# Kernel tuning notes

Measured on AMD Instinct MI355X. Metric: run time of the kernel, lower is better.

Reference implementation:

```python
import jax, jax.numpy as jnp
import numpy as np

N = 20000          # num proposals (nodes)
E = 320000         # num edges
IN = 4096          # roi feature dim
EMB = 200          # glove embed dim
HID = 512          # hidden dim
NH = 8             # heads (conv1)
HC = HID // NH     # 64 per-head channels
NCLS = 151         # VG object classes
NEG_SLOPE = 0.2    # PyG GATConv leaky_relu slope


def setup_inputs() -> dict:
    key = jax.random.key(0)
    ks = jax.random.split(key, 18)
    d_in1 = IN + EMB + 128  # 4424, conv1 input dim
    inp = {
        "roi_features": jax.random.normal(ks[0], (N, IN), jnp.float32),
        "box_info": jax.random.uniform(ks[1], (N, 9), jnp.float32),
        # embedding tables
        "emb1": jax.random.normal(ks[2], (NCLS, EMB), jnp.float32) * 0.02,
        "emb2": jax.random.normal(ks[3], (NCLS, EMB), jnp.float32) * 0.02,
        # bbox MLP 9 -> 32 -> 128
        "bw1": jax.random.normal(ks[4], (9, 32), jnp.float32) / np.sqrt(9),
        "bb1": jnp.zeros((32,), jnp.float32),
        "bw2": jax.random.normal(ks[5], (32, 128), jnp.float32) / np.sqrt(32),
        "bb2": jnp.zeros((128,), jnp.float32),
        # GATConv1: d_in1 -> 8 heads x 64, concat
        "W1": jax.random.normal(ks[6], (d_in1, NH * HC), jnp.float32) / np.sqrt(d_in1),
        "a_src1": jax.random.normal(ks[7], (NH, HC), jnp.float32) * 0.1,
        "a_dst1": jax.random.normal(ks[8], (NH, HC), jnp.float32) * 0.1,
        "bias1": jnp.zeros((NH * HC,), jnp.float32),
        # GATConv2: 512 -> 512, 1 head, concat=False
        "W2": jax.random.normal(ks[9], (HID, HID), jnp.float32) / np.sqrt(HID),
        "a_src2": jax.random.normal(ks[10], (1, HID), jnp.float32) * 0.1,
        "a_dst2": jax.random.normal(ks[11], (1, HID), jnp.float32) * 0.1,
        "bias2": jnp.zeros((HID,), jnp.float32),
        # int inputs
        "obj_labels": jax.random.randint(ks[12], (N,), 0, NCLS, jnp.int32),
        "edge_index": jax.random.randint(ks[13], (2, E), 0, N, jnp.int32),
    }
    return inp


def _segment_softmax(logits, seg, n):
    # logits: [E, H]; softmax over edges sharing the same destination seg id
    m = jax.ops.segment_max(logits, seg, num_segments=n)
    e = jnp.exp(logits - m[seg])
    s = jax.ops.segment_sum(e, seg, num_segments=n)
    return e / (s[seg] + 1e-16)


def _gat_conv(x, src, dst, W, a_src, a_dst, bias, concat):
    # PyG GATConv (self-loops already included in src/dst); dropout off (eval)
    n = x.shape[0]
    H, C = a_src.shape
    h = (x @ W).reshape(n, H, C)                      # [N, H, C]
    al_s = jnp.einsum('nhc,hc->nh', h, a_src)         # [N, H]
    al_d = jnp.einsum('nhc,hc->nh', h, a_dst)
    logits = jax.nn.leaky_relu(al_s[src] + al_d[dst], NEG_SLOPE)  # [E, H]
    alpha = _segment_softmax(logits, dst, n)          # [E, H]
    out = jax.ops.segment_sum(alpha[:, :, None] * h[src], dst, num_segments=n)
    out = out.reshape(n, H * C) if concat else out.mean(axis=1)
    return out + bias


def reference(roi_features, box_info, emb1, emb2, bw1, bb1, bw2, bb2,
              W1, a_src1, a_dst1, bias1, W2, a_src2, a_dst2, bias2,
              obj_labels, edge_index):
    n = roi_features.shape[0]
    # predcls mode: GT labels -> embedding lookup
    obj_embed = emb1[obj_labels]                              # [N, 200]
    pos = jax.nn.relu(box_info @ bw1 + bb1)
    pos = jax.nn.relu(pos @ bw2 + bb2)                        # [N, 128]
    x = jnp.concatenate([roi_features, obj_embed, pos], -1)  # [N, 4424]

    # add self-loops (PyG GATConv default)
    ar = jnp.arange(n, dtype=edge_index.dtype)
    src = jnp.concatenate([edge_index[0], ar])
    dst = jnp.concatenate([edge_index[1], ar])

    edge_f1 = jax.nn.elu(_gat_conv(x, src, dst, W1, a_src1, a_dst1, bias1, True))
    obj_feats = _gat_conv(edge_f1, src, dst, W2, a_src2, a_dst2, bias2, False)

    obj_dists = jax.nn.one_hot(obj_labels, NCLS, dtype=jnp.float32)
    edge_pre_rep = jnp.concatenate([roi_features, obj_feats, emb2[obj_labels]], -1)
    return obj_dists, obj_labels, edge_pre_rep
```

## Files before the change

kernel.cpp:

```cpp
#include <hip/hip_runtime.h>
#include <hip/hip_bf16.h>

#define NNODES 20000
#define NEDGES 320000
#define ETOT   (NEDGES + NNODES)
#define KPADX  4224
#define SK     4
#define KC     (KPADX / SK)
#define MPAD   20096
#define NCLS   151
#define EPRW   4808
#define OUT_LAB_OFF  3020000L
#define OUT_EPR_OFF  3040000L
#define NSLOPE 0.2f

typedef __attribute__((ext_vector_type(8))) short bf16x8;
typedef __attribute__((ext_vector_type(4))) float f32x4;
typedef __attribute__((ext_vector_type(4))) short s16x4;

__device__ __forceinline__ short f2bf(float v) {
  union { __hip_bfloat16 b; short s; } u;
  u.b = __float2bfloat16(v);
  return u.s;
}

__device__ __forceinline__ float bf2f(short s) {
  union { float f; unsigned u; } x;
  x.u = ((unsigned)(unsigned short)s) << 16;
  return x.f;
}

__device__ __forceinline__ void gld16(const short* g, short* l) {
  __builtin_amdgcn_global_load_lds(
      (const __attribute__((address_space(1))) unsigned int*)g,
      (__attribute__((address_space(3))) unsigned int*)l, 16, 0, 0);
}

#define QB0  5000
#define QB0b (QB0 + 10000)
#define QB1  (QB0b + 5000)
#define QB2  (QB1 + 1584)
#define QB3  (QB2 + 2112)
#define QB4  (QB3 + 256)
#define QB5  (QB4 + 1329)
#define QB6  (QB5 + 151)

__global__ __launch_bounds__(256) void mega_prep_kernel(
    const float* __restrict__ roi, const float* __restrict__ box,
    const float* __restrict__ emb1, const float* __restrict__ emb2,
    const float* __restrict__ bw1, const float* __restrict__ bb1,
    const float* __restrict__ bw2, const float* __restrict__ bb2,
    const float* __restrict__ W1, const float* __restrict__ W2,
    const int* __restrict__ labels, const int* __restrict__ ei,
    short* __restrict__ x, short* __restrict__ w1t, short* __restrict__ w2t,
    short* __restrict__ ef1, int* __restrict__ deg,
    float* __restrict__ als2, float* __restrict__ ald2,
    float* __restrict__ E1, float* __restrict__ dout) {
  const int b = blockIdx.x;
  const int tid = threadIdx.x;

  __shared__ float hids[4][32];
  __shared__ float tile[32][33];

  if (b < QB0) {
    const int c0 = b * 2048 + tid;
    f32x4 v0[8], v1[8];
#pragma unroll
    for (int k = 0; k < 8; ++k) {
      const int c = c0 + k * 256;
      const float* src = &roi[((long)(c >> 9) << 12) + (c & 511) * 8];
      v0[k] = *(const f32x4*)src;
      v1[k] = *(const f32x4*)(src + 4);
    }
#pragma unroll
    for (int k = 0; k < 8; ++k) {
      const int c = c0 + k * 256;
      bf16x8 bb;
      bb[0] = f2bf(v0[k].x); bb[1] = f2bf(v0[k].y);
      bb[2] = f2bf(v0[k].z); bb[3] = f2bf(v0[k].w);
      bb[4] = f2bf(v1[k].x); bb[5] = f2bf(v1[k].y);
      bb[6] = f2bf(v1[k].z); bb[7] = f2bf(v1[k].w);
      __builtin_nontemporal_store(bb,
          (bf16x8*)&x[(long)(c >> 9) * KPADX + (c & 511) * 8]);
    }
  } else if (b < QB0b) {
    const int t = b - QB0;
    const int c0 = t * 2048 + tid;
    f32x4 v[8];
#pragma unroll
    for (int k = 0; k < 8; ++k) {
      const int c = c0 + k * 256;
      v[k] = *(const f32x4*)&roi[((long)(c >> 10) << 12) + (c & 1023) * 4];
    }
#pragma unroll
    for (int k = 0; k < 8; ++k) {
      const int c = c0 + k * 256;
      __builtin_nontemporal_store(v[k],
          (f32x4*)&dout[OUT_EPR_OFF + (long)(c >> 10) * EPRW + (c & 1023) * 4]);
    }
  } else if (b < QB1) {
    const int w = tid >> 6;
    const int lane = tid & 63;
    const int nd = (b - QB0b) * 4 + w;
    if (lane < 32) {
      float a = bb1[lane];
#pragma unroll
      for (int i = 0; i < 9; ++i) a += box[nd * 9 + i] * bw1[i * 32 + lane];
      hids[w][lane] = a > 0.f ? a : 0.f;
    }
    __syncthreads();
    const long xrow = (long)nd * KPADX;
#pragma unroll
    for (int jj = 0; jj < 2; ++jj) {
      const int j = lane + jj * 64;
      float a = bb2[j];
#pragma unroll
      for (int i = 0; i < 32; ++i) a += hids[w][i] * bw2[i * 128 + j];
      a = a > 0.f ? a : 0.f;
      x[xrow + 4096 + j] = f2bf(a);
    }
    const int lab = labels[nd];
    float* epr = dout + OUT_EPR_OFF + (long)nd * EPRW;
    if (lane < 50) {
      const f32x4 e2 = *(const f32x4*)&emb2[lab * 200 + lane * 4];
      __builtin_nontemporal_store(e2, (f32x4*)&epr[4608 + lane * 4]);
    }
    for (int j = lane; j < NCLS; j += 64)
      dout[(long)nd * NCLS + j] = (j == lab) ? 1.f : 0.f;
    if (lane == 0) dout[OUT_LAB_OFF + nd] = (float)lab;
  } else if (b < QB2) {
    const int t = (b - QB1) * 256 + tid;
    if (t < 96 * KPADX) x[(long)NNODES * KPADX + t] = 0;
    if (t < 96 * 512)   ef1[(long)NNODES * 512 + t] = 0;
    if (t < MPAD)       { als2[t] = 0.f; ald2[t] = 0.f; }
  } else if (b < QB3) {
    const int t = b - QB2;
    const int n0 = (t % 16) * 32;
    const int k0 = (t / 16) * 32;
    const int tx = tid & 31, ty = tid >> 5;
#pragma unroll
    for (int i = ty; i < 32; i += 8) {
      const int kp = k0 + i;
      const int src = kp < 4096 ? kp : kp + 200;
      tile[i][tx] = W1[(long)src * 512 + (n0 + tx)];
    }
    __syncthreads();
#pragma unroll
    for (int i = ty; i < 32; i += 8)
      w1t[(long)(n0 + i) * KPADX + (k0 + tx)] = f2bf(tile[tx][i]);
  } else if (b < QB4) {
    const int t = b - QB3;
    const int n0 = (t % 16) * 32;
    const int k0 = (t / 16) * 32;
    const int tx = tid & 31, ty = tid >> 5;
#pragma unroll
    for (int i = ty; i < 32; i += 8)
      tile[i][tx] = W2[(long)(k0 + i) * 512 + (n0 + tx)];
    __syncthreads();
#pragma unroll
    for (int i = ty; i < 32; i += 8)
      w2t[(long)(n0 + i) * 512 + (k0 + tx)] = f2bf(tile[tx][i]);
  } else if (b < QB5) {
    const int e = (b - QB4) * 256 + tid;
    if (e < ETOT) {
      const int d = (e < NEDGES) ? ei[NEDGES + e] : (e - NEDGES);
      atomicAdd(&deg[d], 1);
    }
  } else {
    const int c = b - QB5;
#pragma unroll
    for (int jj = 0; jj < 2; ++jj) {
      const int j = tid + jj * 256;
      float a = 0.f;
      for (int k = 0; k < 200; ++k)
        a += emb1[c * 200 + k] * W1[(long)(4096 + k) * 512 + j];
      E1[c * 512 + j] = a;
    }
  }
}

__global__ __launch_bounds__(256) void scan_kernel(const int* __restrict__ deg,
                                                   int* __restrict__ off,
                                                   int* __restrict__ cur) {
  __shared__ int part[256];
  const int tid = threadIdx.x;
  const int chunk = (NNODES + 255) / 256;
  int start = tid * chunk;
  int end = start + chunk; if (end > NNODES) end = NNODES;
  int s = 0;
  for (int i = start; i < end; ++i) s += deg[i];
  part[tid] = s;
  __syncthreads();
  for (int d = 1; d < 256; d <<= 1) {
    const int v = (tid >= d) ? part[tid - d] : 0;
    __syncthreads();
    part[tid] += v;
    __syncthreads();
  }
  int base = part[tid] - s;
  for (int i = start; i < end; ++i) { off[i] = base; cur[i] = base; base += deg[i]; }
}

__global__ void csr_fill_kernel(const int* __restrict__ ei, int* __restrict__ cur,
                                int* __restrict__ csrs) {
  const int e = blockIdx.x * 256 + threadIdx.x;
  if (e >= ETOT) return;
  const int s = (e < NEDGES) ? ei[e] : (e - NEDGES);
  const int d = (e < NEDGES) ? ei[NEDGES + e] : (e - NEDGES);
  unsigned slot = (unsigned)atomicAdd(&cur[d], 1);
  if (slot >= ETOT) slot = 0;
  csrs[slot] = s;
}

__global__ __launch_bounds__(256) void gemm_split(const short* __restrict__ A,
                                                  const short* __restrict__ BT,
                                                  short* __restrict__ hp) {
  __shared__ short As[2][4096];
  __shared__ short Bs[2][4096];
  const int tid = threadIdx.x;
  const int lane = tid & 63;
  const int w = tid >> 6;
  const int wr = w >> 1, wc = w & 1;
  const int wid = (blockIdx.x & 7) * 314 + ((int)blockIdx.x >> 3);
  const long bm = (long)(wid >> 4) * 128;
  const int  sk = (wid >> 2) & 3;
  const long bn = (long)(wid & 3) * 128;

  f32x4 acc[4][4] = {};

  const short* gA0 = A + (bm + w * 32 + (lane >> 2)) * (long)KPADX + sk * KC + (lane & 3) * 8;
  const short* gA1 = gA0 + 16L * KPADX;
  const short* gB0 = BT + (bn + w * 32 + (lane >> 2)) * (long)KPADX + sk * KC + (lane & 3) * 8;
  const short* gB1 = gB0 + 16L * KPADX;

  const int lofs = w * 1024;
  const int ar = (wr * 64 + (lane & 15)) * 32 + (lane >> 4) * 8;
  const int br = (wc * 64 + (lane & 15)) * 32 + (lane >> 4) * 8;

  gld16(gA0, &As[0][lofs]); gld16(gA1, &As[0][lofs + 512]);
  gld16(gB0, &Bs[0][lofs]); gld16(gB1, &Bs[0][lofs + 512]);
  gA0 += 32; gA1 += 32; gB0 += 32; gB1 += 32;

  const int NT = KC / 32;
  int cur = 0;
  for (int t = 0; t < NT; ++t) {
    if (t + 1 < NT) {
      gld16(gA0, &As[cur ^ 1][lofs]); gld16(gA1, &As[cur ^ 1][lofs + 512]);
      gld16(gB0, &Bs[cur ^ 1][lofs]); gld16(gB1, &Bs[cur ^ 1][lofs + 512]);
      gA0 += 32; gA1 += 32; gB0 += 32; gB1 += 32;
      asm volatile("s_waitcnt vmcnt(4)" ::: "memory");
    } else {
      asm volatile("s_waitcnt vmcnt(0)" ::: "memory");
    }
    __builtin_amdgcn_s_barrier();
    bf16x8 a[4], b[4];
#pragma unroll
    for (int mi = 0; mi < 4; ++mi) a[mi] = *(const bf16x8*)&As[cur][ar + mi * 512];
#pragma unroll
    for (int ni = 0; ni < 4; ++ni) b[ni] = *(const bf16x8*)&Bs[cur][br + ni * 512];
#pragma unroll
    for (int mi = 0; mi < 4; ++mi)
#pragma unroll
      for (int ni = 0; ni < 4; ++ni)
        acc[mi][ni] = __builtin_amdgcn_mfma_f32_16x16x32_bf16(a[mi], b[ni], acc[mi][ni], 0, 0, 0);
    __builtin_amdgcn_s_barrier();
    cur ^= 1;
  }

  short* Cp = hp + (long)sk * MPAD * 512;
#pragma unroll
  for (int mi = 0; mi < 4; ++mi) {
#pragma unroll
    for (int ni = 0; ni < 4; ++ni) {
      const long row0 = bm + wr * 64 + mi * 16 + (lane >> 4) * 4;
      const long col  = bn + wc * 64 + ni * 16 + (lane & 15);
#pragma unroll
      for (int r = 0; r < 4; ++r)
        Cp[(row0 + r) * 512 + col] = f2bf(acc[mi][ni][r]);
    }
  }
}

__global__ __launch_bounds__(256) void reduce1_kernel(short* __restrict__ hp,
    const float* __restrict__ E1, const int* __restrict__ labels,
    const float* __restrict__ aS, const float* __restrict__ aD,
    float* __restrict__ als, float* __restrict__ ald) {
  const int row = blockIdx.x * 4 + (threadIdx.x >> 6);
  const int lane = threadIdx.x & 63;
  const int c0 = lane * 8;
  const long base = (long)row * 512 + c0;
  float v[8] = {};
#pragma unroll
  for (int s = 0; s < SK; ++s) {
    const bf16x8 p = *(const bf16x8*)&hp[(long)s * MPAD * 512 + base];
#pragma unroll
    for (int j = 0; j < 8; ++j) v[j] += bf2f(p[j]);
  }
  const int lab = (row < NNODES) ? labels[row] : 0;
  const float* e1r = E1 + (long)lab * 512;
#pragma unroll
  for (int j = 0; j < 8; ++j) v[j] += e1r[c0 + j];
  bf16x8 o;
#pragma unroll
  for (int j = 0; j < 8; ++j) o[j] = f2bf(v[j]);
  *(bf16x8*)&hp[base] = o;
  float s_ = 0.f, d_ = 0.f;
#pragma unroll
  for (int j = 0; j < 8; ++j) {
    s_ += v[j] * aS[c0 + j];
    d_ += v[j] * aD[c0 + j];
  }
#pragma unroll
  for (int oo = 1; oo < 8; oo <<= 1) {
    s_ += __shfl_xor(s_, oo);
    d_ += __shfl_xor(d_, oo);
  }
  if ((lane & 7) == 0) {
    const int head = lane >> 3;
    als[row * 8 + head] = s_;
    ald[row * 8 + head] = d_;
  }
}

__global__ __launch_bounds__(256) void gemm_bt(const short* __restrict__ A,
                                               const short* __restrict__ BT,
                                               short* __restrict__ C,
                                               const float* __restrict__ aS,
                                               const float* __restrict__ aD,
                                               float* __restrict__ als,
                                               float* __restrict__ ald,
                                               int Kpad, int Ncols, int H) {
  __shared__ short As[2][4096];
  __shared__ short Bs[2][4096];
  const int tid = threadIdx.x;
  const int lane = tid & 63;
  const int w = tid >> 6;
  const int wr = w >> 1, wc = w & 1;
  const int nbn = Ncols >> 7;
  const long bm = (long)((int)blockIdx.x / nbn) * 128;
  const long bn = (long)((int)blockIdx.x % nbn) * 128;

  f32x4 acc[4][4] = {};

  const short* gA0 = A + (bm + w * 32 + (lane >> 2)) * (long)Kpad + (lane & 3) * 8;
  const short* gA1 = gA0 + 16L * Kpad;
  const short* gB0 = BT + (bn + w * 32 + (lane >> 2)) * (long)Kpad + (lane & 3) * 8;
  const short* gB1 = gB0 + 16L * Kpad;

  const int lofs = w * 1024;
  const int ar = (wr * 64 + (lane & 15)) * 32 + (lane >> 4) * 8;
  const int br = (wc * 64 + (lane & 15)) * 32 + (lane >> 4) * 8;

  gld16(gA0, &As[0][lofs]); gld16(gA1, &As[0][lofs + 512]);
  gld16(gB0, &Bs[0][lofs]); gld16(gB1, &Bs[0][lofs + 512]);
  gA0 += 32; gA1 += 32; gB0 += 32; gB1 += 32;

  const int NT = Kpad / 32;
  int cur = 0;
  for (int t = 0; t < NT; ++t) {
    if (t + 1 < NT) {
      gld16(gA0, &As[cur ^ 1][lofs]); gld16(gA1, &As[cur ^ 1][lofs + 512]);
      gld16(gB0, &Bs[cur ^ 1][lofs]); gld16(gB1, &Bs[cur ^ 1][lofs + 512]);
      gA0 += 32; gA1 += 32; gB0 += 32; gB1 += 32;
      asm volatile("s_waitcnt vmcnt(4)" ::: "memory");
    } else {
      asm volatile("s_waitcnt vmcnt(0)" ::: "memory");
    }
    __builtin_amdgcn_s_barrier();
    bf16x8 a[4], b[4];
#pragma unroll
    for (int mi = 0; mi < 4; ++mi) a[mi] = *(const bf16x8*)&As[cur][ar + mi * 512];
#pragma unroll
    for (int ni = 0; ni < 4; ++ni) b[ni] = *(const bf16x8*)&Bs[cur][br + ni * 512];
#pragma unroll
    for (int mi = 0; mi < 4; ++mi)
#pragma unroll
      for (int ni = 0; ni < 4; ++ni)
        acc[mi][ni] = __builtin_amdgcn_mfma_f32_16x16x32_bf16(a[mi], b[ni], acc[mi][ni], 0, 0, 0);
    __builtin_amdgcn_s_barrier();
    cur ^= 1;
  }

  const int colb = (int)bn + wc * 64 + (lane & 15);

#pragma unroll
  for (int mi = 0; mi < 4; ++mi) {
#pragma unroll
    for (int ni = 0; ni < 4; ++ni) {
      const long row0 = bm + wr * 64 + mi * 16 + (lane >> 4) * 4;
      const long col  = bn + wc * 64 + ni * 16 + (lane & 15);
#pragma unroll
      for (int r = 0; r < 4; ++r)
        C[(row0 + r) * (long)Ncols + col] = f2bf(acc[mi][ni][r]);
    }
  }

  float asv[4], adv[4];
#pragma unroll
  for (int ni = 0; ni < 4; ++ni) {
    asv[ni] = aS[colb + ni * 16];
    adv[ni] = aD[colb + ni * 16];
  }
  const int head = (H == 8) ? (((int)bn >> 6) + wc) : 0;
#pragma unroll
  for (int mi = 0; mi < 4; ++mi) {
#pragma unroll
    for (int r = 0; r < 4; ++r) {
      float s = 0.f, d = 0.f;
#pragma unroll
      for (int ni = 0; ni < 4; ++ni) {
        const float v = acc[mi][ni][r];
        s += v * asv[ni];
        d += v * adv[ni];
      }
#pragma unroll
      for (int o = 1; o < 16; o <<= 1) {
        s += __shfl_xor(s, o);
        d += __shfl_xor(d, o);
      }
      if ((lane & 15) == 0) {
        const long row = bm + wr * 64 + mi * 16 + (lane >> 4) * 4 + r;
        atomicAdd(&als[row * H + head], s);
        atomicAdd(&ald[row * H + head], d);
      }
    }
  }
}

__global__ __launch_bounds__(256) void gather1_kernel(const int* __restrict__ off,
    const int* __restrict__ csrs,
    const float* __restrict__ als, const float* __restrict__ ald,
    const short* __restrict__ h1, const float* __restrict__ bias,
    short* __restrict__ ef1) {
  const int dn = blockIdx.x * 4 + (threadIdx.x >> 6);
  const int lane = threadIdx.x & 63;
  const int c0 = lane * 8;
  const int head = lane >> 3;
  const int beg = off[dn];
  const int end = (dn == NNODES - 1) ? ETOT : off[dn + 1];
  const float ad = ald[dn * 8 + head];
  float sum = 0.f;
  float acc[8] = {};
  for (int i = beg; i < end; ++i) {
    int s = csrs[i];
    if ((unsigned)s >= NNODES) s = 0;
    float l = als[s * 8 + head] + ad;
    l = l > 0.f ? l : NSLOPE * l;
    const float wgt = expf(l);
    sum += wgt;
    const bf16x8 hv = *(const bf16x8*)&h1[(long)s * 512 + c0];
#pragma unroll
    for (int j = 0; j < 8; ++j) acc[j] += wgt * bf2f(hv[j]);
  }
  const float inv = 1.f / (sum + 1e-16f);
  bf16x8 outv;
#pragma unroll
  for (int j = 0; j < 8; ++j) {
    float r = acc[j] * inv + bias[c0 + j];
    r = r > 0.f ? r : expm1f(r);
    outv[j] = f2bf(r);
  }
  *(bf16x8*)&ef1[(long)dn * 512 + c0] = outv;
}

__global__ __launch_bounds__(256) void gather2_kernel(const int* __restrict__ off,
    const int* __restrict__ csrs,
    const float* __restrict__ als, const float* __restrict__ ald,
    const short* __restrict__ h2, const float* __restrict__ bias,
    float* __restrict__ dout) {
  const int dn = blockIdx.x * 4 + (threadIdx.x >> 6);
  const int lane = threadIdx.x & 63;
  const int c0 = lane * 8;
  const int beg = off[dn];
  const int end = (dn == NNODES - 1) ? ETOT : off[dn + 1];
  const float ad = ald[dn];
  float sum = 0.f;
  float acc[8] = {};
  for (int i = beg; i < end; ++i) {
    int s = csrs[i];
    if ((unsigned)s >= NNODES) s = 0;
    float l = als[s] + ad;
    l = l > 0.f ? l : NSLOPE * l;
    const float wgt = expf(l);
    sum += wgt;
    const bf16x8 hv = *(const bf16x8*)&h2[(long)s * 512 + c0];
#pragma unroll
    for (int j = 0; j < 8; ++j) acc[j] += wgt * bf2f(hv[j]);
  }
  const float inv = 1.f / (sum + 1e-16f);
  float* epr = dout + OUT_EPR_OFF + (long)dn * EPRW + 4096;
  f32x4 o0, o1;
  o0.x = acc[0] * inv + bias[c0 + 0];
  o0.y = acc[1] * inv + bias[c0 + 1];
  o0.z = acc[2] * inv + bias[c0 + 2];
  o0.w = acc[3] * inv + bias[c0 + 3];
  o1.x = acc[4] * inv + bias[c0 + 4];
  o1.y = acc[5] * inv + bias[c0 + 5];
  o1.z = acc[6] * inv + bias[c0 + 6];
  o1.w = acc[7] * inv + bias[c0 + 7];
  __builtin_nontemporal_store(o0, (f32x4*)&epr[c0]);
  __builtin_nontemporal_store(o1, (f32x4*)&epr[c0 + 4]);
}

extern "C" void kernel_launch(void* const* d_in, const int* in_sizes, int n_in,
                              void* d_out, int out_size, void* d_ws, size_t ws_size,
                              hipStream_t stream) {
  const float* roi  = (const float*)d_in[0];
  const float* box  = (const float*)d_in[1];
  const float* emb1 = (const float*)d_in[2];
  const float* emb2 = (const float*)d_in[3];
  const float* bw1  = (const float*)d_in[4];
  const float* bb1  = (const float*)d_in[5];
  const float* bw2  = (const float*)d_in[6];
  const float* bb2  = (const float*)d_in[7];
  const float* W1   = (const float*)d_in[8];
  const float* as1  = (const float*)d_in[9];
  const float* ad1  = (const float*)d_in[10];
  const float* b1   = (const float*)d_in[11];
  const float* W2   = (const float*)d_in[12];
  const float* as2  = (const float*)d_in[13];
  const float* ad2  = (const float*)d_in[14];
  const float* b2   = (const float*)d_in[15];
  const int* labels = (const int*)d_in[16];
  const int* ei     = (const int*)d_in[17];
  float* dout = (float*)d_out;

  char* wsb = (char*)d_ws;
  size_t o = 0;
  auto alloc = [&](size_t bytes) -> void* {
    void* p = wsb + o;
    o += (bytes + 255) & ~(size_t)255;
    return p;
  };
  short* x    = (short*)alloc((size_t)MPAD * KPADX * 2);
  short* w1t  = (short*)alloc((size_t)512 * KPADX * 2);
  short* hp   = (short*)alloc((size_t)SK * MPAD * 512 * 2);
  short* h1   = hp;
  short* ef1  = (short*)alloc((size_t)MPAD * 512 * 2);
  short* w2t  = (short*)alloc((size_t)512 * 512 * 2);
  short* h2   = (short*)alloc((size_t)MPAD * 512 * 2);
  float* als1 = (float*)alloc((size_t)MPAD * 8 * 4);
  float* ald1 = (float*)alloc((size_t)MPAD * 8 * 4);
  float* als2 = (float*)alloc((size_t)MPAD * 4);
  float* ald2 = (float*)alloc((size_t)MPAD * 4);
  float* E1   = (float*)alloc((size_t)NCLS * 512 * 4);
  int*   deg  = (int*)alloc((size_t)NNODES * 4);
  int*   offs = (int*)alloc((size_t)NNODES * 4);
  int*   cur  = (int*)alloc((size_t)NNODES * 4);
  int*   csrs = (int*)alloc((size_t)ETOT * 4);

  const int EB = (ETOT + 255) / 256;

  hipMemsetAsync(deg, 0, (size_t)NNODES * 4, stream);

  hipLaunchKernelGGL(mega_prep_kernel, dim3(QB6), dim3(256), 0, stream,
                     roi, box, emb1, emb2, bw1, bb1, bw2, bb2, W1, W2,
                     labels, ei, x, w1t, w2t, ef1, deg,
                     als2, ald2, E1, dout);
  hipLaunchKernelGGL(scan_kernel, dim3(1), dim3(256), 0, stream, deg, offs, cur);
  hipLaunchKernelGGL(csr_fill_kernel, dim3(EB), dim3(256), 0, stream, ei, cur, csrs);
  hipLaunchKernelGGL(gemm_split, dim3(157 * SK * 4), dim3(256), 0, stream,
                     x, w1t, hp);
  hipLaunchKernelGGL(reduce1_kernel, dim3(MPAD / 4), dim3(256), 0, stream,
                     hp, E1, labels, as1, ad1, als1, ald1);
  hipLaunchKernelGGL(gather1_kernel, dim3(NNODES / 4), dim3(256), 0, stream,
                     offs, csrs, als1, ald1, h1, b1, ef1);
  hipLaunchKernelGGL(gemm_bt, dim3(157 * 4), dim3(256), 0, stream,
                     ef1, w2t, h2, as2, ad2, als2, ald2, 512, 512, 1);
  hipLaunchKernelGGL(gather2_kernel, dim3(NNODES / 4), dim3(256), 0, stream,
                     offs, csrs, als2, ald2, h2, b2, dout);
}
```

Before: 621.2 us.

## Fuse roi copy with bf16 cast and XOR-swizzle GEMM LDS tiles

The prep kernel now reads each roi float4 once and writes it both to the fp32 output slice and as bf16 into the padded x matrix. Before, two separate block ranges each read roi. The two GEMM kernels apply an XOR swizzle to the 16-byte chunk positions in LDS, on both the global-to-LDS load side and the fragment read side, to cut LDS bank conflicts. The fused path swaps 16-byte bf16 stores for 8-byte stores, and the swizzle has to stay consistent between writer and reader lanes.

After: 577.6 us. -7.0%, faster.

```diff
diff --git a/kernel.cpp b/kernel.cpp
--- a/kernel.cpp
+++ b/kernel.cpp
@@ -36,14 +36,13 @@
       (__attribute__((address_space(3))) unsigned int*)l, 16, 0, 0);
 }
 
-#define QB0  5000
-#define QB0b (QB0 + 10000)
-#define QB1  (QB0b + 5000)
-#define QB2  (QB1 + 1584)
-#define QB3  (QB2 + 2112)
-#define QB4  (QB3 + 256)
-#define QB5  (QB4 + 1329)
-#define QB6  (QB5 + 151)
+#define QB0 10000
+#define QB1 (QB0 + 5000)
+#define QB2 (QB1 + 1584)
+#define QB3 (QB2 + 2112)
+#define QB4 (QB3 + 256)
+#define QB5 (QB4 + 1329)
+#define QB6 (QB5 + 151)
 
 __global__ __launch_bounds__(256) void mega_prep_kernel(
     const float* __restrict__ roi, const float* __restrict__ box,
@@ -63,45 +62,26 @@
   __shared__ float tile[32][33];
 
   if (b < QB0) {
-    const int c0 = b * 2048 + tid;
-    f32x4 v0[8], v1[8];
+    const int base = b * 2048 + tid;
+    f32x4 v[8];
+#pragma unroll
+    for (int k = 0; k < 8; ++k)
+      v[k] = *(const f32x4*)&roi[(long)(base + k * 256) * 4];
 #pragma unroll
     for (int k = 0; k < 8; ++k) {
-      const int c = c0 + k * 256;
-      const float* src = &roi[((long)(c >> 9) << 12) + (c & 511) * 8];
-      v0[k] = *(const f32x4*)src;
-      v1[k] = *(const f32x4*)(src + 4);
-    }
-#pragma unroll
-    for (int k = 0; k < 8; ++k) {
-      const int c = c0 + k * 256;
-      bf16x8 bb;
-      bb[0] = f2bf(v0[k].x); bb[1] = f2bf(v0[k].y);
-      bb[2] = f2bf(v0[k].z); bb[3] = f2bf(v0[k].w);
-      bb[4] = f2bf(v1[k].x); bb[5] = f2bf(v1[k].y);
-      bb[6] = f2bf(v1[k].z); bb[7] = f2bf(v1[k].w);
-      __builtin_nontemporal_store(bb,
-          (bf16x8*)&x[(long)(c >> 9) * KPADX + (c & 511) * 8]);
-    }
-  } else if (b < QB0b) {
-    const int t = b - QB0;
-    const int c0 = t * 2048 + tid;
-    f32x4 v[8];
-#pragma unroll
-    for (int k = 0; k < 8; ++k) {
-      const int c = c0 + k * 256;
-      v[k] = *(const f32x4*)&roi[((long)(c >> 10) << 12) + (c & 1023) * 4];
-    }
-#pragma unroll
-    for (int k = 0; k < 8; ++k) {
-      const int c = c0 + k * 256;
+      const int t = base + k * 256;
+      const int node = t >> 10, cq = t & 1023;
       __builtin_nontemporal_store(v[k],
-          (f32x4*)&dout[OUT_EPR_OFF + (long)(c >> 10) * EPRW + (c & 1023) * 4]);
+          (f32x4*)&dout[OUT_EPR_OFF + (long)node * EPRW + cq * 4]);
+      s16x4 bb;
+      bb.x = f2bf(v[k].x); bb.y = f2bf(v[k].y);
+      bb.z = f2bf(v[k].z); bb.w = f2bf(v[k].w);
+      *(s16x4*)&x[(long)node * KPADX + cq * 4] = bb;
     }
   } else if (b < QB1) {
     const int w = tid >> 6;
     const int lane = tid & 63;
-    const int nd = (b - QB0b) * 4 + w;
+    const int nd = (b - QB0) * 4 + w;
     if (lane < 32) {
       float a = bb1[lane];
 #pragma unroll
@@ -228,14 +208,16 @@
 
   f32x4 acc[4][4] = {};
 
-  const short* gA0 = A + (bm + w * 32 + (lane >> 2)) * (long)KPADX + sk * KC + (lane & 3) * 8;
+  const int ksw = ((lane & 3) ^ ((lane >> 3) & 3)) * 8;
+  const short* gA0 = A + (bm + w * 32 + (lane >> 2)) * (long)KPADX + sk * KC + ksw;
   const short* gA1 = gA0 + 16L * KPADX;
-  const short* gB0 = BT + (bn + w * 32 + (lane >> 2)) * (long)KPADX + sk * KC + (lane & 3) * 8;
+  const short* gB0 = BT + (bn + w * 32 + (lane >> 2)) * (long)KPADX + sk * KC + ksw;
   const short* gB1 = gB0 + 16L * KPADX;
 
   const int lofs = w * 1024;
-  const int ar = (wr * 64 + (lane & 15)) * 32 + (lane >> 4) * 8;
-  const int br = (wc * 64 + (lane & 15)) * 32 + (lane >> 4) * 8;
+  const int sw = ((lane >> 4) ^ (((lane & 15) >> 1) & 3)) * 8;
+  const int ar = (wr * 64 + (lane & 15)) * 32 + sw;
+  const int br = (wc * 64 + (lane & 15)) * 32 + sw;
 
   gld16(gA0, &As[0][lofs]); gld16(gA1, &As[0][lofs + 512]);
   gld16(gB0, &Bs[0][lofs]); gld16(gB1, &Bs[0][lofs + 512]);
@@ -342,14 +324,16 @@
 
   f32x4 acc[4][4] = {};
 
-  const short* gA0 = A + (bm + w * 32 + (lane >> 2)) * (long)Kpad + (lane & 3) * 8;
+  const int ksw = ((lane & 3) ^ ((lane >> 3) & 3)) * 8;
+  const short* gA0 = A + (bm + w * 32 + (lane >> 2)) * (long)Kpad + ksw;
   const short* gA1 = gA0 + 16L * Kpad;
-  const short* gB0 = BT + (bn + w * 32 + (lane >> 2)) * (long)Kpad + (lane & 3) * 8;
+  const short* gB0 = BT + (bn + w * 32 + (lane >> 2)) * (long)Kpad + ksw;
   const short* gB1 = gB0 + 16L * Kpad;
 
   const int lofs = w * 1024;
-  const int ar = (wr * 64 + (lane & 15)) * 32 + (lane >> 4) * 8;
-  const int br = (wc * 64 + (lane & 15)) * 32 + (lane >> 4) * 8;
+  const int sw = ((lane >> 4) ^ (((lane & 15) >> 1) & 3)) * 8;
+  const int ar = (wr * 64 + (lane & 15)) * 32 + sw;
+  const int br = (wc * 64 + (lane & 15)) * 32 + sw;
 
   gld16(gA0, &As[0][lofs]); gld16(gA1, &As[0][lofs + 512]);
   gld16(gB0, &Bs[0][lofs]); gld16(gB1, &Bs[0][lofs + 512]);
```
